# Kernel optimization log

Hardware: AMD Instinct MI355X
Metric: run time of the kernel (lower is better)

Reference implementation:

```python
import jax, jax.numpy as jnp
import numpy as np

EPS = 1e-6

def setup_inputs() -> dict:
    key = jax.random.key(0)
    ks = jax.random.split(key, 9)
    B, H, M = 8192, 1024, 16
    Hh = H // 2
    s = lambda k, shape, fan: jax.random.normal(k, shape, jnp.float32) * (1.0 / np.sqrt(fan))
    return {
        "query_embedding": jax.random.normal(ks[0], (B, H), jnp.float32),
        "cls1_w": s(ks[1], (Hh, H), H),
        "cls1_b": jnp.zeros((Hh,), jnp.float32),
        "cls3_w": s(ks[2], (M, Hh), Hh),
        "cls3_b": jnp.zeros((M,), jnp.float32),
        "exp_w1": s(ks[3], (M, Hh, H), H),
        "exp_b1": jnp.zeros((M, Hh), jnp.float32),
        "exp_w2": s(ks[4], (M, H, Hh), Hh),
        "exp_b2": jnp.zeros((M, H), jnp.float32),
    }

def _l2_normalize(x, eps=EPS):
    # F.normalize: x / clamp(||x||_2, min=eps)
    n = jnp.sqrt(jnp.sum(x * x, axis=-1, keepdims=True))
    return x / jnp.maximum(n, eps)

def reference(query_embedding, cls1_w, cls1_b, cls3_w, cls3_b,
              exp_w1, exp_b1, exp_w2, exp_b2):
    q = query_embedding  # [B, H]
    # --- cls(): gating network (eval, sbmoe_top1) ---
    x1 = jax.nn.relu(q @ cls1_w.T + cls1_b)          # [B, H/2]
    logits = x1 @ cls3_w.T + cls3_b                  # [B, M]
    probs = jax.nn.softmax(logits, axis=-1)          # [B, M]
    top1 = jnp.argmax(probs, axis=-1)                # [B]
    mask = jax.nn.one_hot(top1, probs.shape[-1], dtype=probs.dtype)
    gates = probs * mask                             # [B, M] (one nonzero/row)
    # --- query_embedder(): run all experts, gate, combine ---
    h = jax.nn.relu(jnp.einsum('bd,mhd->bmh', q, exp_w1) + exp_b1)   # [B, M, H/2]
    expert_out = jnp.einsum('bmh,mdh->bmd', h, exp_w2) + exp_b2      # [B, M, H]
    combined = jnp.einsum('bmd,bm->bd', expert_out, gates)           # [B, H]
    out = _l2_normalize(combined) + q
    return out
```

## Files before the change

### kernel.cpp

```cpp
#include <hip/hip_runtime.h>
#include <math.h>

#define NB 8192
#define H 1024
#define HH 512
#define NEXP 16
#define NT128 96
#define AMBIG_THR 1e-3f

typedef __attribute__((ext_vector_type(8))) short bfrag;
typedef __attribute__((ext_vector_type(4))) float f4;

__device__ __forceinline__ f4 MF(bfrag a, bfrag b, f4 c) {
    return __builtin_amdgcn_mfma_f32_16x16x32_bf16(a, b, c, 0, 0, 0);
}
__device__ __forceinline__ unsigned short f2bf(float f) {
    unsigned u = __float_as_uint(f);
    u += 0x7fff + ((u >> 16) & 1);
    return (unsigned short)(u >> 16);
}
__device__ __forceinline__ float bf2f(unsigned short h) {
    return __uint_as_float((unsigned)h << 16);
}

typedef __attribute__((address_space(1))) const unsigned GAS;
typedef __attribute__((address_space(3))) unsigned LAS;
__device__ __forceinline__ void gld16(const void* g, void* l) {
    __builtin_amdgcn_global_load_lds((GAS*)g, (LAS*)l, 16, 0, 0);
}

__global__ __launch_bounds__(256) void cvtA_kernel(
    const float* __restrict__ q, const float* __restrict__ w1, const float* __restrict__ w3,
    unsigned short* __restrict__ qhi, unsigned short* __restrict__ qlo,
    unsigned short* __restrict__ w1hi, unsigned short* __restrict__ w1lo,
    unsigned short* __restrict__ w3hi, unsigned short* __restrict__ w3lo,
    int* __restrict__ counts, int* __restrict__ ambig_cnt)
{
    const int b = blockIdx.x, t = threadIdx.x;
    if (b == 0) {
        if (t < NEXP) counts[t] = 0;
        if (t == NEXP) ambig_cnt[0] = 0;
    }
    const float* src; unsigned short *hi, *lo; int i;
    if (b < 8192)      { src = q;  hi = qhi;  lo = qlo;  i = b * 256 + t; }
    else if (b < 8704) { src = w1; hi = w1hi; lo = w1lo; i = (b - 8192) * 256 + t; }
    else               { src = w3; hi = w3hi; lo = w3lo; i = (b - 8704) * 256 + t; }
    float4 v = ((const float4*)src)[i];
    ushort4 h, l;
    h.x = f2bf(v.x); l.x = f2bf(v.x - bf2f(h.x));
    h.y = f2bf(v.y); l.y = f2bf(v.y - bf2f(h.y));
    h.z = f2bf(v.z); l.z = f2bf(v.z - bf2f(h.z));
    h.w = f2bf(v.w); l.w = f2bf(v.w - bf2f(h.w));
    ((ushort4*)hi)[i] = h;
    ((ushort4*)lo)[i] = l;
}

__global__ __launch_bounds__(256) void cvtB_kernel(
    const float* __restrict__ ew1, const float* __restrict__ ew2,
    unsigned short* __restrict__ d1, unsigned short* __restrict__ d2)
{
    const int b = blockIdx.x, t = threadIdx.x;
    const float* src; unsigned short* dst; int i;
    if (b < 8192) { src = ew1; dst = d1; i = b * 256 + t; }
    else          { src = ew2; dst = d2; i = (b - 8192) * 256 + t; }
    float4 v = ((const float4*)src)[i];
    ushort4 h;
    h.x = f2bf(v.x); h.y = f2bf(v.y); h.z = f2bf(v.z); h.w = f2bf(v.w);
    ((ushort4*)dst)[i] = h;
}

__global__ __launch_bounds__(256) void g1_kernel(
    const unsigned short* __restrict__ qhi, const unsigned short* __restrict__ qlo,
    const unsigned short* __restrict__ w1hi, const unsigned short* __restrict__ w1lo,
    const float* __restrict__ b1,
    unsigned short* __restrict__ x1hi, unsigned short* __restrict__ x1lo)
{
    __shared__ unsigned short Ah[2][128][32];
    __shared__ unsigned short Al[2][128][32];
    __shared__ unsigned short Bh[2][64][32];
    __shared__ unsigned short Bl[2][64][32];

    const int t = threadIdx.x, w = t >> 6, lane = t & 63;
    const int quad = lane >> 4, l16 = lane & 15;
    const int rowA0 = blockIdx.x * 128;
    const int colB0 = blockIdx.y * 64;
    const int rl = lane >> 2, sl = lane & 3;

    const unsigned short* gsrc[6];
    unsigned short* lbase[6];
    int bstr[6];
    #pragma unroll
    for (int j = 0; j < 6; ++j) {
        int c = w + j * 4;
        int rloc; const unsigned short* s; unsigned short* d; int str;
        if (c < 8)       { rloc = c * 16 + rl;        s = qhi  + (size_t)(rowA0 + rloc) * H; d = &Ah[0][c * 16][0];        str = 128 * 32; }
        else if (c < 16) { rloc = (c - 8) * 16 + rl;  s = qlo  + (size_t)(rowA0 + rloc) * H; d = &Al[0][(c - 8) * 16][0];  str = 128 * 32; }
        else if (c < 20) { rloc = (c - 16) * 16 + rl; s = w1hi + (size_t)(colB0 + rloc) * H; d = &Bh[0][(c - 16) * 16][0]; str = 64 * 32; }
        else             { rloc = (c - 20) * 16 + rl; s = w1lo + (size_t)(colB0 + rloc) * H; d = &Bl[0][(c - 20) * 16][0]; str = 64 * 32; }
        int f = (rloc & 3) ^ ((rloc >> 2) & 3);
        gsrc[j]  = s + (sl ^ f) * 8;
        lbase[j] = d;
        bstr[j]  = str;
    }

    const f4 z4 = {0.f, 0.f, 0.f, 0.f};
    f4 acc[2][4] = {{z4, z4, z4, z4}, {z4, z4, z4, z4}};
    const int sw = (quad ^ (l16 & 3) ^ (l16 >> 2)) * 8;
    const int ra0 = w * 32 + l16, ra1 = ra0 + 16;

    auto STAGE = [&](int buf, int kt) {
        #pragma unroll
        for (int j = 0; j < 6; ++j)
            gld16(gsrc[j] + kt * 32, lbase[j] + buf * bstr[j]);
    };
    auto COMPUTE = [&](int buf) {
        bfrag ah0 = *(const bfrag*)&Ah[buf][ra0][sw];
        bfrag al0 = *(const bfrag*)&Al[buf][ra0][sw];
        bfrag ah1 = *(const bfrag*)&Ah[buf][ra1][sw];
        bfrag al1 = *(const bfrag*)&Al[buf][ra1][sw];
        #pragma unroll
        for (int cb = 0; cb < 4; ++cb) {
            bfrag bh = *(const bfrag*)&Bh[buf][cb * 16 + l16][sw];
            bfrag bl = *(const bfrag*)&Bl[buf][cb * 16 + l16][sw];
            acc[0][cb] = MF(al0, bh, MF(ah0, bl, MF(ah0, bh, acc[0][cb])));
            acc[1][cb] = MF(al1, bh, MF(ah1, bl, MF(ah1, bh, acc[1][cb])));
        }
    };

    STAGE(0, 0);
    __syncthreads();
    int cur = 0;
    for (int kt = 1; kt < 32; ++kt) {
        STAGE(cur ^ 1, kt);
        COMPUTE(cur);
        __syncthreads();
        cur ^= 1;
    }
    COMPUTE(cur);

    const int row0 = rowA0 + w * 32;
    #pragma unroll
    for (int cb = 0; cb < 4; ++cb) {
        int col = colB0 + cb * 16 + l16;
        float bias = b1[col];
        #pragma unroll
        for (int rb = 0; rb < 2; ++rb)
            #pragma unroll
            for (int i = 0; i < 4; ++i) {
                int row = rb * 16 + quad * 4 + i;
                float v = fmaxf(acc[rb][cb][i] + bias, 0.f);
                unsigned short hh = f2bf(v);
                size_t idx = (size_t)(row0 + row) * HH + col;
                x1hi[idx] = hh;
                x1lo[idx] = f2bf(v - bf2f(hh));
            }
    }
}

__global__ __launch_bounds__(256) void logits_kernel(
    const unsigned short* __restrict__ x1hi, const unsigned short* __restrict__ x1lo,
    const unsigned short* __restrict__ w3hi, const unsigned short* __restrict__ w3lo,
    const float* __restrict__ b3,
    int* __restrict__ top1, float* __restrict__ gval, int* __restrict__ counts,
    int* __restrict__ ambig_rows, int* __restrict__ ambig_cnt)
{
    __shared__ float lgp[4][32][NEXP];
    const int t = threadIdx.x, wave = t >> 6, lane = t & 63;
    const int quad = lane >> 4, l16 = lane & 15;
    const int row0 = blockIdx.x * 32;
    const f4 z4 = {0.f, 0.f, 0.f, 0.f};

    f4 l0 = z4, l1 = z4;
    const size_t ar0 = (size_t)(row0 + l16) * HH + quad * 8;
    const size_t ar1 = ar0 + (size_t)16 * HH;
    const size_t br = (size_t)l16 * HH + quad * 8;
    #pragma unroll
    for (int ks = 0; ks < 4; ++ks) {
        int kk = wave * 128 + ks * 32;
        bfrag ah0 = *(const bfrag*)(x1hi + ar0 + kk);
        bfrag al0 = *(const bfrag*)(x1lo + ar0 + kk);
        bfrag ah1 = *(const bfrag*)(x1hi + ar1 + kk);
        bfrag al1 = *(const bfrag*)(x1lo + ar1 + kk);
        bfrag bh  = *(const bfrag*)(w3hi + br + kk);
        bfrag bl  = *(const bfrag*)(w3lo + br + kk);
        l0 = MF(al0, bh, MF(ah0, bl, MF(ah0, bh, l0)));
        l1 = MF(al1, bh, MF(ah1, bl, MF(ah1, bh, l1)));
    }
    #pragma unroll
    for (int i = 0; i < 4; ++i) {
        lgp[wave][quad * 4 + i][l16] = l0[i];
        lgp[wave][16 + quad * 4 + i][l16] = l1[i];
    }
    __syncthreads();

    if (t < 32) {
        float lg[NEXP];
        #pragma unroll
        for (int m = 0; m < NEXP; ++m)
            lg[m] = lgp[0][t][m] + lgp[1][t][m] + lgp[2][t][m] + lgp[3][t][m] + b3[m];
        float best = lg[0], second = -3.4e38f; int bi = 0;
        #pragma unroll
        for (int m = 1; m < NEXP; ++m) {
            float v = lg[m];
            if (v > best) { second = best; best = v; bi = m; }
            else if (v > second) second = v;
        }
        float se = 0.f;
        #pragma unroll
        for (int m = 0; m < NEXP; ++m) se += expf(lg[m] - best);
        int grow = row0 + t;
        top1[grow] = bi;
        gval[grow] = 1.f / se;
        atomicAdd(&counts[bi], 1);
        if (best - second < AMBIG_THR) {
            int pos = atomicAdd(ambig_cnt, 1);
            if (pos < NB) ambig_rows[pos] = grow;
        }
    }
}

__global__ __launch_bounds__(256) void fixup1_kernel(
    const float* __restrict__ q, const float* __restrict__ w1, const float* __restrict__ b1,
    const int* __restrict__ ambig_rows, const int* __restrict__ ambig_cnt,
    float* __restrict__ x1buf)
{
    __shared__ __align__(16) float qrow[H];
    const int t = threadIdx.x, wv = t >> 6, ln = t & 63;
    const int chunk = blockIdx.x & 7;
    const int slot  = blockIdx.x >> 3;
    const int base  = chunk * 64;
    int nn = *ambig_cnt; if (nn > NB) nn = NB;
    for (int ii = slot; ii < nn; ii += 32) {
        int row = ambig_rows[ii];
        ((float4*)qrow)[t] = ((const float4*)(q + (size_t)row * H))[t];
        __syncthreads();
        for (int c = base + wv * 2; c < base + 64; c += 8) {
            const float4* w0 = (const float4*)(w1 + (size_t)c * H);
            const float4* w1r = (const float4*)(w1 + (size_t)(c + 1) * H);
            const float4* qv = (const float4*)qrow;
            float s0 = 0.f, s1 = 0.f;
            #pragma unroll
            for (int j = 0; j < 4; ++j) {
                float4 a = qv[j * 64 + ln];
                float4 b0 = w0[j * 64 + ln];
                float4 b1v = w1r[j * 64 + ln];
                s0 += a.x * b0.x + a.y * b0.y + a.z * b0.z + a.w * b0.w;
                s1 += a.x * b1v.x + a.y * b1v.y + a.z * b1v.z + a.w * b1v.w;
            }
            #pragma unroll
            for (int off = 32; off; off >>= 1) {
                s0 += __shfl_xor(s0, off, 64);
                s1 += __shfl_xor(s1, off, 64);
            }
            if (ln == 0) {
                x1buf[(size_t)ii * HH + c]     = fmaxf(s0 + b1[c], 0.f);
                x1buf[(size_t)ii * HH + c + 1] = fmaxf(s1 + b1[c + 1], 0.f);
            }
        }
        __syncthreads();
    }
}

__global__ __launch_bounds__(256) void fixup2_kernel(
    const float* __restrict__ x1buf,
    const float* __restrict__ w3, const float* __restrict__ b3,
    const int* __restrict__ ambig_rows, const int* __restrict__ ambig_cnt,
    int* __restrict__ top1, float* __restrict__ gval, int* __restrict__ counts)
{
    __shared__ float lgs[NEXP];
    const int t = threadIdx.x, wv = t >> 6, ln = t & 63;
    int nn = *ambig_cnt; if (nn > NB) nn = NB;
    for (int ii = blockIdx.x; ii < nn; ii += gridDim.x) {
        int row = ambig_rows[ii];
        const float4* xv = (const float4*)(x1buf + (size_t)ii * HH);
        for (int m = wv; m < NEXP; m += 4) {
            const float4* wr = (const float4*)(w3 + (size_t)m * HH);
            float s = 0.f;
            #pragma unroll
            for (int j = 0; j < 2; ++j) {
                float4 a = xv[j * 64 + ln];
                float4 b = wr[j * 64 + ln];
                s += a.x * b.x + a.y * b.y + a.z * b.z + a.w * b.w;
            }
            #pragma unroll
            for (int off = 32; off; off >>= 1) s += __shfl_xor(s, off, 64);
            if (ln == 0) lgs[m] = s + b3[m];
        }
        __syncthreads();
        if (t == 0) {
            float best = lgs[0]; int bi = 0;
            #pragma unroll
            for (int m = 1; m < NEXP; ++m) if (lgs[m] > best) { best = lgs[m]; bi = m; }
            float se = 0.f;
            #pragma unroll
            for (int m = 0; m < NEXP; ++m) se += expf(lgs[m] - best);
            int old = top1[row];
            if (bi != old) {
                atomicSub(&counts[old], 1);
                atomicAdd(&counts[bi], 1);
                top1[row] = bi;
            }
            gval[row] = 1.f / se;
        }
        __syncthreads();
    }
}

__global__ __launch_bounds__(64) void offsets_kernel(
    const int* __restrict__ counts, int* __restrict__ offsets, int* __restrict__ bpos,
    int* __restrict__ tm_e, int* __restrict__ tm_p, int* __restrict__ tm_end)
{
    if (threadIdx.x == 0) {
        int run = 0;
        for (int e = 0; e < NEXP; ++e) { offsets[e] = run; bpos[e] = run; run += counts[e]; }
        int tile = 0;
        for (int e = 0; e < NEXP; ++e) {
            int beg = offsets[e], end = beg + counts[e];
            for (int p = beg; p < end; p += 128) {
                tm_e[tile] = e; tm_p[tile] = p; tm_end[tile] = end; ++tile;
            }
        }
        for (; tile < NT128; ++tile) tm_e[tile] = -1;
    }
}

__global__ __launch_bounds__(256) void scatter_kernel(
    const int* __restrict__ top1, int* __restrict__ bpos, int* __restrict__ brows)
{
    int b = blockIdx.x * 256 + threadIdx.x;
    int e = top1[b];
    int pos = atomicAdd(&bpos[e], 1);
    brows[pos] = b;
}

__global__ __launch_bounds__(256) void exp1_kernel(
    const unsigned short* __restrict__ qb, const unsigned short* __restrict__ ew1b,
    const float* __restrict__ eb1,
    const int* __restrict__ tm_e, const int* __restrict__ tm_p, const int* __restrict__ tm_end,
    const int* __restrict__ brows, unsigned short* __restrict__ h)
{
    const int e = tm_e[blockIdx.x];
    if (e < 0) return;
    const int p0 = tm_p[blockIdx.x], end = tm_end[blockIdx.x];

    __shared__ unsigned short A[2][128][32];
    __shared__ unsigned short B[2][64][32];

    const int t = threadIdx.x, w = t >> 6, lane = t & 63;
    const int quad = lane >> 4, l16 = lane & 15;
    const int c0 = blockIdx.y * 64;
    const unsigned short* w1p = ew1b + (size_t)e * HH * H;
    const int rl = lane >> 2, sl = lane & 3;

    const unsigned short* gsrc[3];
    unsigned short* lbase[3];
    int bstr[3];
    #pragma unroll
    for (int j = 0; j < 3; ++j) {
        int c = w + j * 4;
        int rloc; const unsigned short* s; unsigned short* d; int str;
        if (c < 8) {
            rloc = c * 16 + rl;
            int pa = p0 + rloc; if (pa >= end) pa = end - 1;
            s = qb + (size_t)brows[pa] * H;
            d = &A[0][c * 16][0]; str = 128 * 32;
        } else {
            rloc = (c - 8) * 16 + rl;
            s = w1p + (size_t)(c0 + rloc) * H;
            d = &B[0][(c - 8) * 16][0]; str = 64 * 32;
        }
        int f = (rloc & 3) ^ ((rloc >> 2) & 3);
        gsrc[j]  = s + (sl ^ f) * 8;
        lbase[j] = d;
        bstr[j]  = str;
    }

    const f4 z4 = {0.f, 0.f, 0.f, 0.f};
    f4 acc[2][4] = {{z4, z4, z4, z4}, {z4, z4, z4, z4}};
    const int sw = (quad ^ (l16 & 3) ^ (l16 >> 2)) * 8;
    const int ra0 = w * 32 + l16, ra1 = ra0 + 16;

    auto STAGE = [&](int buf, int kt) {
        #pragma unroll
        for (int j = 0; j < 3; ++j)
            gld16(gsrc[j] + kt * 32, lbase[j] + buf * bstr[j]);
    };
    auto COMPUTE = [&](int buf) {
        bfrag a0 = *(const bfrag*)&A[buf][ra0][sw];
        bfrag a1 = *(const bfrag*)&A[buf][ra1][sw];
        #pragma unroll
        for (int cb = 0; cb < 4; ++cb) {
            bfrag bb = *(const bfrag*)&B[buf][cb * 16 + l16][sw];
            acc[0][cb] = MF(a0, bb, acc[0][cb]);
            acc[1][cb] = MF(a1, bb, acc[1][cb]);
        }
    };

    STAGE(0, 0);
    __syncthreads();
    int cur = 0;
    for (int kt = 1; kt < 32; ++kt) {
        STAGE(cur ^ 1, kt);
        COMPUTE(cur);
        __syncthreads();
        cur ^= 1;
    }
    COMPUTE(cur);

    const int prow0 = p0 + w * 32;
    #pragma unroll
    for (int cb = 0; cb < 4; ++cb) {
        int col = c0 + cb * 16 + l16;
        float bias = eb1[e * HH + col];
        #pragma unroll
        for (int rb = 0; rb < 2; ++rb)
            #pragma unroll
            for (int i = 0; i < 4; ++i) {
                int row = rb * 16 + quad * 4 + i;
                if (prow0 + row < end)
                    h[(size_t)(prow0 + row) * HH + col] = f2bf(fmaxf(acc[rb][cb][i] + bias, 0.f));
            }
    }
}

__global__ __launch_bounds__(256) void exp2_kernel(
    const unsigned short* __restrict__ h, const unsigned short* __restrict__ ew2b,
    const float* __restrict__ eb2,
    const int* __restrict__ tm_e, const int* __restrict__ tm_p, const int* __restrict__ tm_end,
    const int* __restrict__ brows,
    float* __restrict__ vout, float* __restrict__ psum)
{
    const int e = tm_e[blockIdx.x];
    if (e < 0) return;
    const int p0 = tm_p[blockIdx.x], end = tm_end[blockIdx.x];

    __shared__ unsigned short A[2][128][32];
    __shared__ unsigned short B[2][64][32];

    const int t = threadIdx.x, w = t >> 6, lane = t & 63;
    const int quad = lane >> 4, l16 = lane & 15;
    const int cg = blockIdx.y;
    const int c0 = cg * 64;
    const unsigned short* w2p = ew2b + (size_t)e * H * HH;
    const int rl = lane >> 2, sl = lane & 3;

    const unsigned short* gsrc[3];
    unsigned short* lbase[3];
    int bstr[3];
    #pragma unroll
    for (int j = 0; j < 3; ++j) {
        int c = w + j * 4;
        int rloc; const unsigned short* s; unsigned short* d; int str;
        if (c < 8) {
            rloc = c * 16 + rl;
            int pa = p0 + rloc; if (pa >= end) pa = end - 1;
            s = h + (size_t)pa * HH;
            d = &A[0][c * 16][0]; str = 128 * 32;
        } else {
            rloc = (c - 8) * 16 + rl;
            s = w2p + (size_t)(c0 + rloc) * HH;
            d = &B[0][(c - 8) * 16][0]; str = 64 * 32;
        }
        int f = (rloc & 3) ^ ((rloc >> 2) & 3);
        gsrc[j]  = s + (sl ^ f) * 8;
        lbase[j] = d;
        bstr[j]  = str;
    }

    const f4 z4 = {0.f, 0.f, 0.f, 0.f};
    f4 acc[2][4] = {{z4, z4, z4, z4}, {z4, z4, z4, z4}};
    const int sw = (quad ^ (l16 & 3) ^ (l16 >> 2)) * 8;
    const int ra0 = w * 32 + l16, ra1 = ra0 + 16;

    auto STAGE = [&](int buf, int kt) {
        #pragma unroll
        for (int j = 0; j < 3; ++j)
            gld16(gsrc[j] + kt * 32, lbase[j] + buf * bstr[j]);
    };
    auto COMPUTE = [&](int buf) {
        bfrag a0 = *(const bfrag*)&A[buf][ra0][sw];
        bfrag a1 = *(const bfrag*)&A[buf][ra1][sw];
        #pragma unroll
        for (int cb = 0; cb < 4; ++cb) {
            bfrag bb = *(const bfrag*)&B[buf][cb * 16 + l16][sw];
            acc[0][cb] = MF(a0, bb, acc[0][cb]);
            acc[1][cb] = MF(a1, bb, acc[1][cb]);
        }
    };

    STAGE(0, 0);
    __syncthreads();
    int cur = 0;
    for (int kt = 1; kt < 16; ++kt) {
        STAGE(cur ^ 1, kt);
        COMPUTE(cur);
        __syncthreads();
        cur ^= 1;
    }
    COMPUTE(cur);

    const int pw0 = p0 + w * 32;
    float rs0[4] = {0.f, 0.f, 0.f, 0.f}, rs1[4] = {0.f, 0.f, 0.f, 0.f};
    #pragma unroll
    for (int i = 0; i < 4; ++i) {
        int row0i = quad * 4 + i, row1i = 16 + quad * 4 + i;
        int g0 = pw0 + row0i; if (g0 >= end) g0 = end - 1;
        int g1 = pw0 + row1i; if (g1 >= end) g1 = end - 1;
        int gr0 = brows[g0], gr1 = brows[g1];
        #pragma unroll
        for (int cb = 0; cb < 4; ++cb) {
            int col = c0 + cb * 16 + l16;
            float bias = eb2[e * H + col];
            float v0 = acc[0][cb][i] + bias;
            float v1 = acc[1][cb][i] + bias;
            vout[(size_t)gr0 * H + col] = v0;
            vout[(size_t)gr1 * H + col] = v1;
            rs0[i] += v0 * v0;
            rs1[i] += v1 * v1;
        }
    }
    #pragma unroll
    for (int i = 0; i < 4; ++i) {
        float s0 = rs0[i], s1 = rs1[i];
        #pragma unroll
        for (int off = 8; off; off >>= 1) {
            s0 += __shfl_xor(s0, off, 16);
            s1 += __shfl_xor(s1, off, 16);
        }
        if (l16 == 0) {
            int g0 = pw0 + quad * 4 + i;      if (g0 >= end) g0 = end - 1;
            int g1 = pw0 + 16 + quad * 4 + i; if (g1 >= end) g1 = end - 1;
            psum[(size_t)brows[g0] * 16 + cg] = s0;
            psum[(size_t)brows[g1] * 16 + cg] = s1;
        }
    }
}

__global__ __launch_bounds__(256) void finalize_kernel(
    float* __restrict__ out, const float* __restrict__ q,
    const float* __restrict__ psum, const float* __restrict__ gval)
{
    const int row = blockIdx.x, t = threadIdx.x;
    float s = 0.f;
    #pragma unroll
    for (int j = 0; j < 16; ++j) s += psum[(size_t)row * 16 + j];
    float g = gval[row];
    float sc = g / fmaxf(g * sqrtf(s), 1e-6f);
    size_t i = (size_t)row * 256 + t;
    float4 v = ((const float4*)out)[i];
    float4 qq = ((const float4*)q)[i];
    float4 o;
    o.x = v.x * sc + qq.x;
    o.y = v.y * sc + qq.y;
    o.z = v.z * sc + qq.z;
    o.w = v.w * sc + qq.w;
    ((float4*)out)[i] = o;
}

extern "C" void kernel_launch(void* const* d_in, const int* in_sizes, int n_in,
                              void* d_out, int out_size, void* d_ws, size_t ws_size,
                              hipStream_t stream) {
    const float* q      = (const float*)d_in[0];
    const float* cls1_w = (const float*)d_in[1];
    const float* cls1_b = (const float*)d_in[2];
    const float* cls3_w = (const float*)d_in[3];
    const float* cls3_b = (const float*)d_in[4];
    const float* exp_w1 = (const float*)d_in[5];
    const float* exp_b1 = (const float*)d_in[6];
    const float* exp_w2 = (const float*)d_in[7];
    const float* exp_b2 = (const float*)d_in[8];
    float* out = (float*)d_out;

    char* w = (char*)d_ws;
    float* psum   = (float*)w;              w += (size_t)NB * 16 * 4;
    float* gvalp  = (float*)w;              w += (size_t)NB * 4;
    int* top1     = (int*)w;                w += (size_t)NB * 4;
    int* brows    = (int*)w;                w += (size_t)NB * 4;
    int* ambig_rows = (int*)w;              w += (size_t)NB * 4;
    int* counts   = (int*)w;                w += 16 * 4;
    int* offsets  = (int*)w;                w += 16 * 4;
    int* bpos     = (int*)w;                w += 16 * 4;
    int* ambig_cnt = (int*)w;               w += 4 * 4;
    int* tm_e     = (int*)w;                w += NT128 * 4;
    int* tm_p     = (int*)w;                w += NT128 * 4;
    int* tm_end   = (int*)w;                w += NT128 * 4;
    w = (char*)(((size_t)w + 15) & ~(size_t)15);
    unsigned short* qhi  = (unsigned short*)w;  w += (size_t)NB * H * 2;
    unsigned short* qlo  = (unsigned short*)w;  w += (size_t)NB * H * 2;
    unsigned short* x1hi = (unsigned short*)w;
    unsigned short* x1lo = x1hi + (size_t)NB * HH;  w += (size_t)NB * HH * 2 * 2;
    unsigned short* hbuf = (unsigned short*)w;  w += (size_t)NB * HH * 2;
    unsigned short* w1hi = (unsigned short*)w;  w += (size_t)HH * H * 2;
    unsigned short* w1lo = (unsigned short*)w;  w += (size_t)HH * H * 2;
    unsigned short* w3hi = (unsigned short*)w;  w += (size_t)NEXP * HH * 2;
    unsigned short* w3lo = (unsigned short*)w;  w += (size_t)NEXP * HH * 2;
    unsigned short* ew1b = x1hi;
    unsigned short* ew2b = qlo;
    float* x1buf = (float*)x1hi;

    cvtA_kernel<<<8712, 256, 0, stream>>>(q, cls1_w, cls3_w, qhi, qlo, w1hi, w1lo,
                                          w3hi, w3lo, counts, ambig_cnt);
    g1_kernel<<<dim3(NB / 128, 8), 256, 0, stream>>>(qhi, qlo, w1hi, w1lo, cls1_b, x1hi, x1lo);
    logits_kernel<<<NB / 32, 256, 0, stream>>>(x1hi, x1lo, w3hi, w3lo, cls3_b,
                                               top1, gvalp, counts, ambig_rows, ambig_cnt);
    fixup1_kernel<<<256, 256, 0, stream>>>(q, cls1_w, cls1_b, ambig_rows, ambig_cnt, x1buf);
    fixup2_kernel<<<64, 256, 0, stream>>>(x1buf, cls3_w, cls3_b, ambig_rows, ambig_cnt,
                                          top1, gvalp, counts);
    cvtB_kernel<<<16384, 256, 0, stream>>>(exp_w1, exp_w2, ew1b, ew2b);
    offsets_kernel<<<1, 64, 0, stream>>>(counts, offsets, bpos, tm_e, tm_p, tm_end);
    scatter_kernel<<<NB / 256, 256, 0, stream>>>(top1, bpos, brows);
    exp1_kernel<<<dim3(NT128, 8), 256, 0, stream>>>(qhi, ew1b, exp_b1,
                                                    tm_e, tm_p, tm_end, brows, hbuf);
    exp2_kernel<<<dim3(NT128, 16), 256, 0, stream>>>(hbuf, ew2b, exp_b2,
                                                     tm_e, tm_p, tm_end, brows, out, psum);
    finalize_kernel<<<NB, 256, 0, stream>>>(out, q, psum, gvalp);
}
```

Before: 381.7 us.

## Triple-buffer GEMM staging with vmcnt waits and fuse offsets/scatter kernels

The three MFMA GEMM kernels move from double-buffered LDS staging with two syncthreads per step to a three-stage ring. Each step waits with a partial s_waitcnt vmcnt, so two tiles of global-to-LDS loads stay in flight behind compute, and it uses a single barrier per iteration. The offsets and scatter kernels are merged into one single-block kernel that keeps the bucket cursors in shared-memory atomics, removing one launch. The costs are more LDS per block, which may lower occupancy, and a serial 8192-row scatter inside one block.

```diff
diff --git a/kernel.cpp b/kernel.cpp
--- a/kernel.cpp
+++ b/kernel.cpp
@@ -75,10 +75,10 @@
     const float* __restrict__ b1,
     unsigned short* __restrict__ x1hi, unsigned short* __restrict__ x1lo)
 {
-    __shared__ unsigned short Ah[2][128][32];
-    __shared__ unsigned short Al[2][128][32];
-    __shared__ unsigned short Bh[2][64][32];
-    __shared__ unsigned short Bl[2][64][32];
+    __shared__ unsigned short Ah[3][128][32];
+    __shared__ unsigned short Al[3][128][32];
+    __shared__ unsigned short Bh[3][64][32];
+    __shared__ unsigned short Bl[3][64][32];
 
     const int t = threadIdx.x, w = t >> 6, lane = t & 63;
     const int quad = lane >> 4, l16 = lane & 15;
@@ -128,15 +128,14 @@
     };
 
     STAGE(0, 0);
-    __syncthreads();
-    int cur = 0;
-    for (int kt = 1; kt < 32; ++kt) {
-        STAGE(cur ^ 1, kt);
-        COMPUTE(cur);
-        __syncthreads();
-        cur ^= 1;
-    }
-    COMPUTE(cur);
+    STAGE(1, 1);
+    for (int kt = 0; kt < 32; ++kt) {
+        if (kt < 31) asm volatile("s_waitcnt vmcnt(6)" ::: "memory");
+        else         asm volatile("s_waitcnt vmcnt(0)" ::: "memory");
+        __builtin_amdgcn_s_barrier();
+        if (kt < 30) STAGE((kt + 2) % 3, kt + 2);
+        COMPUTE(kt % 3);
+    }
 
     const int row0 = rowA0 + w * 32;
     #pragma unroll
@@ -306,31 +305,31 @@
     }
 }
 
-__global__ __launch_bounds__(64) void offsets_kernel(
-    const int* __restrict__ counts, int* __restrict__ offsets, int* __restrict__ bpos,
-    int* __restrict__ tm_e, int* __restrict__ tm_p, int* __restrict__ tm_end)
-{
-    if (threadIdx.x == 0) {
-        int run = 0;
-        for (int e = 0; e < NEXP; ++e) { offsets[e] = run; bpos[e] = run; run += counts[e]; }
-        int tile = 0;
+__global__ __launch_bounds__(256) void osc_kernel(
+    const int* __restrict__ counts,
+    int* __restrict__ tm_e, int* __restrict__ tm_p, int* __restrict__ tm_end,
+    const int* __restrict__ top1, int* __restrict__ brows)
+{
+    __shared__ int sbpos[NEXP];
+    const int t = threadIdx.x;
+    if (t == 0) {
+        int run = 0, tile = 0;
         for (int e = 0; e < NEXP; ++e) {
-            int beg = offsets[e], end = beg + counts[e];
+            sbpos[e] = run;
+            int beg = run, end = run + counts[e];
             for (int p = beg; p < end; p += 128) {
                 tm_e[tile] = e; tm_p[tile] = p; tm_end[tile] = end; ++tile;
             }
+            run = end;
         }
         for (; tile < NT128; ++tile) tm_e[tile] = -1;
     }
-}
-
-__global__ __launch_bounds__(256) void scatter_kernel(
-    const int* __restrict__ top1, int* __restrict__ bpos, int* __restrict__ brows)
-{
-    int b = blockIdx.x * 256 + threadIdx.x;
-    int e = top1[b];
-    int pos = atomicAdd(&bpos[e], 1);
-    brows[pos] = b;
+    __syncthreads();
+    for (int i = t; i < NB; i += 256) {
+        int e = top1[i];
+        int pos = atomicAdd(&sbpos[e], 1);
+        brows[pos] = i;
+    }
 }
 
 __global__ __launch_bounds__(256) void exp1_kernel(
@@ -343,8 +342,8 @@
     if (e < 0) return;
     const int p0 = tm_p[blockIdx.x], end = tm_end[blockIdx.x];
 
-    __shared__ unsigned short A[2][128][32];
-    __shared__ unsigned short B[2][64][32];
+    __shared__ unsigned short A[3][128][32];
+    __shared__ unsigned short B[3][64][32];
 
     const int t = threadIdx.x, w = t >> 6, lane = t & 63;
     const int quad = lane >> 4, l16 = lane & 15;
@@ -397,15 +396,14 @@
     };
 
     STAGE(0, 0);
-    __syncthreads();
-    int cur = 0;
-    for (int kt = 1; kt < 32; ++kt) {
-        STAGE(cur ^ 1, kt);
-        COMPUTE(cur);
-        __syncthreads();
-        cur ^= 1;
-    }
-    COMPUTE(cur);
+    STAGE(1, 1);
+    for (int kt = 0; kt < 32; ++kt) {
+        if (kt < 31) asm volatile("s_waitcnt vmcnt(3)" ::: "memory");
+        else         asm volatile("s_waitcnt vmcnt(0)" ::: "memory");
+        __builtin_amdgcn_s_barrier();
+        if (kt < 30) STAGE((kt + 2) % 3, kt + 2);
+        COMPUTE(kt % 3);
+    }
 
     const int prow0 = p0 + w * 32;
     #pragma unroll
@@ -434,8 +432,8 @@
     if (e < 0) return;
     const int p0 = tm_p[blockIdx.x], end = tm_end[blockIdx.x];
 
-    __shared__ unsigned short A[2][128][32];
-    __shared__ unsigned short B[2][64][32];
+    __shared__ unsigned short A[3][128][32];
+    __shared__ unsigned short B[3][64][32];
 
     const int t = threadIdx.x, w = t >> 6, lane = t & 63;
     const int quad = lane >> 4, l16 = lane & 15;
@@ -489,15 +487,14 @@
     };
 
     STAGE(0, 0);
-    __syncthreads();
-    int cur = 0;
-    for (int kt = 1; kt < 16; ++kt) {
-        STAGE(cur ^ 1, kt);
-        COMPUTE(cur);
-        __syncthreads();
-        cur ^= 1;
-    }
-    COMPUTE(cur);
+    STAGE(1, 1);
+    for (int kt = 0; kt < 16; ++kt) {
+        if (kt < 15) asm volatile("s_waitcnt vmcnt(3)" ::: "memory");
+        else         asm volatile("s_waitcnt vmcnt(0)" ::: "memory");
+        __builtin_amdgcn_s_barrier();
+        if (kt < 14) STAGE((kt + 2) % 3, kt + 2);
+        COMPUTE(kt % 3);
+    }
 
     const int pw0 = p0 + w * 32;
     float rs0[4] = {0.f, 0.f, 0.f, 0.f}, rs1[4] = {0.f, 0.f, 0.f, 0.f};
@@ -597,6 +594,7 @@
     unsigned short* ew1b = x1hi;
     unsigned short* ew2b = qlo;
     float* x1buf = (float*)x1hi;
+    (void)offsets; (void)bpos;
 
     cvtA_kernel<<<8712, 256, 0, stream>>>(q, cls1_w, cls3_w, qhi, qlo, w1hi, w1lo,
                                           w3hi, w3lo, counts, ambig_cnt);
@@ -607,8 +605,7 @@
     fixup2_kernel<<<64, 256, 0, stream>>>(x1buf, cls3_w, cls3_b, ambig_rows, ambig_cnt,
                                           top1, gvalp, counts);
     cvtB_kernel<<<16384, 256, 0, stream>>>(exp_w1, exp_w2, ew1b, ew2b);
-    offsets_kernel<<<1, 64, 0, stream>>>(counts, offsets, bpos, tm_e, tm_p, tm_end);
-    scatter_kernel<<<NB / 256, 256, 0, stream>>>(top1, bpos, brows);
+    osc_kernel<<<1, 256, 0, stream>>>(counts, tm_e, tm_p, tm_end, top1, brows);
     exp1_kernel<<<dim3(NT128, 8), 256, 0, stream>>>(qhi, ew1b, exp_b1,
                                                     tm_e, tm_p, tm_end, brows, hbuf);
     exp2_kernel<<<dim3(NT128, 16), 256, 0, stream>>>(hbuf, ew2b, exp_b2,
```

After: 356.6 us. 1.07x faster.
